# Performance work log

Measured on AMD Instinct MI355X. Metric: run time of the kernel, lower is better.

## Reference

```python
import jax, jax.numpy as jnp
import numpy as np

E, H, D = 512, 8, 64
B, T = 2, 1024
HD = H * D


def _linear(x, W, b):
    return x @ W + b


def _ln(x, g, b):
    mu = x.mean(-1, keepdims=True)
    var = ((x - mu) ** 2).mean(-1, keepdims=True)
    return (x - mu) / jnp.sqrt(var + 1e-5) * g + b


def _l2norm(x):
    n = jnp.sqrt((x * x).sum(-1, keepdims=True))
    return x / jnp.maximum(n, 1e-12)


def setup_inputs() -> dict:
    key = jax.random.key(0)
    ks = jax.random.split(key, 32)
    s = 0.02
    inp = {
        'x': jax.random.normal(ks[0], (B, T, E), jnp.float32),
        'b_min': jax.random.normal(ks[1], (B, T, E), jnp.float32),
        'b_max': jax.random.normal(ks[2], (B, T, E), jnp.float32),
        'motif_context': jax.random.normal(ks[3], (B, T, E), jnp.float32),
        'Wk': jax.random.normal(ks[4], (E, HD), jnp.float32) * s,
        'bk': jnp.zeros((HD,), jnp.float32),
        'Wq': jax.random.normal(ks[5], (E, HD), jnp.float32) * s,
        'bq': jnp.zeros((HD,), jnp.float32),
        'Wv': jax.random.normal(ks[6], (E, HD), jnp.float32) * s,
        'bv': jnp.zeros((HD,), jnp.float32),
        'Wo': jax.random.normal(ks[7], (HD, E), jnp.float32) * s,
        'bo': jnp.zeros((E,), jnp.float32),
        'Wd': jax.random.normal(ks[8], (E, H), jnp.float32) * s,
        'bd': jnp.zeros((H,), jnp.float32),
        'Wgw': jax.random.normal(ks[9], (E, H), jnp.float32) * s,
        'bgw': jnp.zeros((H,), jnp.float32),
        'Wgf': jax.random.normal(ks[10], (E, H), jnp.float32) * s,
        'bgf': jnp.zeros((H,), jnp.float32),
        'Wps': jax.random.normal(ks[11], (E, E), jnp.float32) * s,
        'bps': jnp.zeros((E,), jnp.float32),
        'ln1_g': jnp.ones((E,), jnp.float32),
        'ln1_b': jnp.zeros((E,), jnp.float32),
        'ln2_g': jnp.ones((E,), jnp.float32),
        'ln2_b': jnp.zeros((E,), jnp.float32),
        'W1': jax.random.normal(ks[12], (E, 4 * E), jnp.float32) * s,
        'b1': jnp.zeros((4 * E,), jnp.float32),
        'W2': jax.random.normal(ks[13], (4 * E, E), jnp.float32) * s,
        'b2': jnp.zeros((E,), jnp.float32),
    }
    return inp


def reference(x, b_min, b_max, motif_context,
              Wk, bk, Wq, bq, Wv, bv, Wo, bo, Wd, bd,
              Wgw, bgw, Wgf, bgf, Wps, bps,
              ln1_g, ln1_b, ln2_g, ln2_b, W1, b1, W2, b2):
    Bs, Ts, Es = x.shape
    x_n = _ln(x, ln1_g, ln1_b)
    k = _l2norm(_linear(x_n, Wk, bk).reshape(Bs, Ts, H, D))
    q = _l2norm(_linear(x_n, Wq, bq).reshape(Bs, Ts, H, D))
    v = jnp.tanh(_linear(x_n, Wv, bv).reshape(Bs, Ts, H, D))
    d = jax.nn.softplus(_linear(x_n, Wd, bd))            # (B,T,H)
    gw = jax.nn.sigmoid(_linear(x_n, Wgw, bgw)) ** 2     # (B,T,H)
    gf = 1.0 - jax.nn.sigmoid(_linear(x_n, Wgf, bgf)) ** 2

    # gated linear recurrent scan via cumsum of rank-1 updates
    v_gated = v * (d * gw)[..., None]                    # (B,T,H,D)
    updates = jnp.einsum('bthi,bthj->bthij', v_gated, k)  # (B,T,H,D,D)
    decay = jnp.clip(d * gf, 1e-6, 0.999)
    log_decay = jnp.log(decay)[..., None, None]          # (B,T,H,1,1)
    exp_cum_decay = jnp.exp(jnp.cumsum(log_decay, axis=1))
    state = jnp.cumsum(updates / (exp_cum_decay + 1e-8), axis=1) * exp_cum_decay
    readout = jnp.einsum('bthij,bthj->bthi', state, q)   # (B,T,H,D)
    next_mem = state[:, -1]

    x2 = x + _linear(readout.reshape(Bs, Ts, HD), Wo, bo) + 0.1 * motif_context
    h = _ln(x2, ln2_g, ln2_b)
    x3 = x2 + _linear(jax.nn.gelu(_linear(h, W1, b1), approximate=False), W2, b2)
    probe = _linear(x3, Wps, bps)
    return (x3, next_mem, b_min + probe, b_max + probe)
```

## Files before the change

kernel.cpp:

```cpp
#include <hip/hip_runtime.h>


typedef unsigned short u16;
typedef unsigned int u32;
typedef __attribute__((ext_vector_type(8))) short short8;
typedef __attribute__((ext_vector_type(4))) float floatx4;

__device__ __forceinline__ float b2f(u16 u) {
  u32 x = ((u32)u) << 16;
  return __uint_as_float(x);
}
__device__ __forceinline__ u16 f2b(float f) {
  u32 x = __float_as_uint(f);
  u32 r = (x + 0x7fffu + ((x >> 16) & 1u)) >> 16;
  return (u16)r;
}
__device__ __forceinline__ float4 b4_to_f4(uint2 u) {
  float4 r;
  r.x = __uint_as_float((u.x & 0xffffu) << 16);
  r.y = __uint_as_float(u.x & 0xffff0000u);
  r.z = __uint_as_float((u.y & 0xffffu) << 16);
  r.w = __uint_as_float(u.y & 0xffff0000u);
  return r;
}

__device__ __forceinline__ void stage16(const u16* g, u16* lds_wave_base) {
  __builtin_amdgcn_global_load_lds((const __attribute__((address_space(1))) void*)g,
                                   (__attribute__((address_space(3))) void*)lds_wave_base,
                                   16, 0, 0);
}

template <int ROWS>
__device__ __forceinline__ void stage_tile64(const u16* __restrict__ G, int ldK, int kb,
                                             u16* lds, int tid) {
#pragma unroll
  for (int r = 0; r < ROWS / 32; ++r) {
    int slot = r * 256 + tid;
    int row = slot >> 3;
    int kwg = (slot & 7) ^ (row & 7);
    stage16(G + (size_t)row * ldK + kb * 64 + kwg * 8,
            lds + (size_t)(r * 256 + (tid >> 6) * 64) * 8);
  }
}

__device__ __forceinline__ void ln_row(const float* __restrict__ xr,
                                       const float* __restrict__ g,
                                       const float* __restrict__ bt,
                                       u16* __restrict__ yr, int tid, float* red) {
  float x0 = xr[tid], x1 = xr[tid + 256];
  float s = x0 + x1, ss = x0 * x0 + x1 * x1;
#pragma unroll
  for (int o = 32; o > 0; o >>= 1) { s += __shfl_xor(s, o); ss += __shfl_xor(ss, o); }
  if ((tid & 63) == 0) { red[tid >> 6] = s; red[4 + (tid >> 6)] = ss; }
  __syncthreads();
  float ts = red[0] + red[1] + red[2] + red[3];
  float tss = red[4] + red[5] + red[6] + red[7];
  float mu = ts * (1.f / 512.f);
  float var = tss * (1.f / 512.f) - mu * mu;
  float rstd = 1.0f / sqrtf(var + 1e-5f);
  yr[tid] = f2b((x0 - mu) * rstd * g[tid] + bt[tid]);
  yr[tid + 256] = f2b((x1 - mu) * rstd * g[tid + 256] + bt[tid + 256]);
}

__global__ __launch_bounds__(256) void prep_weights(
    const float* __restrict__ Wk, const float* __restrict__ Wq,
    const float* __restrict__ Wv, const float* __restrict__ Wo,
    const float* __restrict__ Wps, const float* __restrict__ W1,
    const float* __restrict__ W2, const float* __restrict__ Wd,
    const float* __restrict__ Wgw, const float* __restrict__ Wgf,
    const float* __restrict__ bk, const float* __restrict__ bq,
    const float* __restrict__ bv, const float* __restrict__ bd,
    const float* __restrict__ bgw, const float* __restrict__ bgf,
    const float* __restrict__ x, const float* __restrict__ ln1g,
    const float* __restrict__ ln1b,
    u16* __restrict__ WTQ, u16* __restrict__ WTO, u16* __restrict__ WTPS,
    u16* __restrict__ WT1, u16* __restrict__ WT2, float* __restrict__ BQV,
    u16* __restrict__ XN) {
  int bid = blockIdx.x, tid = threadIdx.x;
  __shared__ float tile[32][33];
  __shared__ float red[8];
  if (bid < 3328) {
    const float* src;
    u16* dst;
    int C, rel, tiles_x;
    if (bid < 256)       { src = Wk;  dst = WTQ;           C = 512;  rel = bid;        tiles_x = 16; }
    else if (bid < 512)  { src = Wq;  dst = WTQ + 262144;  C = 512;  rel = bid - 256;  tiles_x = 16; }
    else if (bid < 768)  { src = Wv;  dst = WTQ + 524288;  C = 512;  rel = bid - 512;  tiles_x = 16; }
    else if (bid < 1024) { src = Wo;  dst = WTO;           C = 512;  rel = bid - 768;  tiles_x = 16; }
    else if (bid < 1280) { src = Wps; dst = WTPS;          C = 512;  rel = bid - 1024; tiles_x = 16; }
    else if (bid < 2304) { src = W1;  dst = WT1;           C = 2048; rel = bid - 1280; tiles_x = 64; }
    else                 { src = W2;  dst = WT2;           C = 512;  rel = bid - 2304; tiles_x = 16; }
    int R = (bid >= 1280 && bid < 2304) ? 512 : (bid >= 2304 ? 2048 : 512);
    int c0 = (rel % tiles_x) * 32, r0 = (rel / tiles_x) * 32;
    int tx = tid & 31, ty = tid >> 5;
#pragma unroll
    for (int i = 0; i < 4; ++i)
      tile[ty + i * 8][tx] = src[(size_t)(r0 + ty + i * 8) * C + c0 + tx];
    __syncthreads();
#pragma unroll
    for (int i = 0; i < 4; ++i)
      dst[(size_t)(c0 + ty + i * 8) * R + r0 + tx] = f2b(tile[tx][ty + i * 8]);
  } else if (bid < 3392) {
    int idx = (bid - 3328) * 256 + tid;
    const int stride = 64 * 256;
    for (int i = idx; i < 128 * 512; i += stride) {
      int local = i >> 9, k = i & 511;
      float v = 0.f;
      if (local < 8) v = Wd[k * 8 + local];
      else if (local < 16) v = Wgw[k * 8 + (local - 8)];
      else if (local < 24) v = Wgf[k * 8 + (local - 16)];
      WTQ[(size_t)(1536 + local) * 512 + k] = f2b(v);
    }
    for (int i = idx; i < 1664; i += stride) {
      float v = 0.f;
      if (i < 512) v = bk[i];
      else if (i < 1024) v = bq[i - 512];
      else if (i < 1536) v = bv[i - 1024];
      else if (i < 1544) v = bd[i - 1536];
      else if (i < 1552) v = bgw[i - 1544];
      else if (i < 1560) v = bgf[i - 1552];
      BQV[i] = v;
    }
  } else {
    int row = bid - 3392;
    ln_row(x + (size_t)row * 512, ln1g, ln1b, XN + (size_t)row * 512, tid, red);
  }
}

__global__ __launch_bounds__(256) void ln_f32(const float* __restrict__ X,
                                              const float* __restrict__ g,
                                              const float* __restrict__ bt,
                                              u16* __restrict__ Y) {
  __shared__ float red[8];
  ln_row(X + (size_t)blockIdx.x * 512, g, bt, Y + (size_t)blockIdx.x * 512,
         threadIdx.x, red);
}

template <int BM, int EPI>
__global__ __launch_bounds__(256, (BM == 64 ? 4 : 6)) void gemm2s(
    const u16* __restrict__ A, const u16* __restrict__ BT, const float* __restrict__ bias,
    float* __restrict__ outf, float* __restrict__ outf2, u16* __restrict__ outb,
    u16* __restrict__ outb2, u16* __restrict__ outb3,
    const float* __restrict__ aux0, const float* __restrict__ aux1, int M, int N, int K) {
  constexpr int MT = BM / 32;
  constexpr int S = BM / 32 + 2;
  __shared__ __align__(16) u16 As[2][BM * 64];
  __shared__ __align__(16) u16 Bs[2][64 * 64];
  __shared__ float ssb[2][BM];
  const int tid = threadIdx.x;
  const int lane = tid & 63, wave = tid >> 6;
  const int wm = wave >> 1, wn = wave & 1;
  const int m0 = blockIdx.y * BM, n0 = blockIdx.x * 64;
  floatx4 acc[MT][2] = {};
  const int fr = lane & 15, kq = lane >> 4;
  const int nk = K >> 6;
  const u16* Ab = A + (size_t)m0 * K;
  const u16* Bb = BT + (size_t)n0 * K;

  stage_tile64<BM>(Ab, K, 0, As[0], tid);
  stage_tile64<64>(Bb, K, 0, Bs[0], tid);

  for (int kb = 0; kb < nk; ++kb) {
    const int cur = kb & 1;
    if (kb + 1 < nk) {
      stage_tile64<BM>(Ab, K, kb + 1, As[cur ^ 1], tid);
      stage_tile64<64>(Bb, K, kb + 1, Bs[cur ^ 1], tid);
      if constexpr (S == 4) asm volatile("s_waitcnt vmcnt(4)" ::: "memory");
      else asm volatile("s_waitcnt vmcnt(3)" ::: "memory");
    } else {
      asm volatile("s_waitcnt vmcnt(0)" ::: "memory");
    }
    asm volatile("s_barrier" ::: "memory");

#pragma unroll
    for (int sub = 0; sub < 2; ++sub) {
      short8 af[MT], bf[2];
#pragma unroll
      for (int mt = 0; mt < MT; ++mt) {
        int row = wm * (BM / 2) + mt * 16 + fr;
        int c = sub * 4 + kq;
        af[mt] = *(const short8*)&As[cur][row * 64 + ((c ^ (row & 7)) << 3)];
      }
#pragma unroll
      for (int nt = 0; nt < 2; ++nt) {
        int row = wn * 32 + nt * 16 + fr;
        int c = sub * 4 + kq;
        bf[nt] = *(const short8*)&Bs[cur][row * 64 + ((c ^ (row & 7)) << 3)];
      }
#pragma unroll
      for (int mt = 0; mt < MT; ++mt)
#pragma unroll
        for (int nt = 0; nt < 2; ++nt)
          acc[mt][nt] =
              __builtin_amdgcn_mfma_f32_16x16x32_bf16(af[mt], bf[nt], acc[mt][nt], 0, 0, 0);
    }
    asm volatile("s_waitcnt lgkmcnt(0)" ::: "memory");
    asm volatile("s_barrier" ::: "memory");
  }

  const int col = lane & 15;
  const int rbase = (lane >> 4) * 4;

  float vv[MT][2][4];
#pragma unroll
  for (int nt = 0; nt < 2; ++nt) {
    int gc = n0 + wn * 32 + nt * 16 + col;
    float bvv = bias[gc];
#pragma unroll
    for (int mt = 0; mt < MT; ++mt)
#pragma unroll
      for (int r = 0; r < 4; ++r) vv[mt][nt][r] = acc[mt][nt][r] + bvv;
  }

  if constexpr (EPI == 5) {
    const int sec = n0 >> 9;
    const int h = (n0 & 511) >> 6;
    if (sec == 3) {
#pragma unroll
      for (int nt = 0; nt < 2; ++nt) {
        int gcl = (n0 - 1536) + wn * 32 + nt * 16 + col;
#pragma unroll
        for (int mt = 0; mt < MT; ++mt) {
          int gr = m0 + wm * (BM / 2) + mt * 16 + rbase;
#pragma unroll
          for (int r = 0; r < 4; ++r)
            outf[(size_t)(gr + r) * 128 + gcl] = vv[mt][nt][r];
        }
      }
    } else if (sec == 2) {
#pragma unroll
      for (int nt = 0; nt < 2; ++nt) {
        int d = wn * 32 + nt * 16 + col;
#pragma unroll
        for (int mt = 0; mt < MT; ++mt) {
          int gr = m0 + wm * (BM / 2) + mt * 16 + rbase;
#pragma unroll
          for (int r = 0; r < 4; ++r) {
            int tok = gr + r;
            int bh = (tok >> 10) * 8 + h;
            outb3[((size_t)bh * 1024 + (tok & 1023)) * 64 + d] = f2b(tanhf(vv[mt][nt][r]));
          }
        }
      }
    } else {
#pragma unroll
      for (int mt = 0; mt < MT; ++mt) {
#pragma unroll
        for (int r = 0; r < 4; ++r) {
          float ss = vv[mt][0][r] * vv[mt][0][r] + vv[mt][1][r] * vv[mt][1][r];
          ss += __shfl_xor(ss, 1);
          ss += __shfl_xor(ss, 2);
          ss += __shfl_xor(ss, 4);
          ss += __shfl_xor(ss, 8);
          if ((lane & 15) == 0)
            ssb[wn][wm * (BM / 2) + mt * 16 + rbase + r] = ss;
        }
      }
      __syncthreads();
      u16* dst = (sec == 0) ? outb : outb2;
#pragma unroll
      for (int mt = 0; mt < MT; ++mt) {
#pragma unroll
        for (int r = 0; r < 4; ++r) {
          int br = wm * (BM / 2) + mt * 16 + rbase + r;
          float tot = ssb[0][br] + ssb[1][br];
          float rs = 1.0f / fmaxf(sqrtf(tot), 1e-12f);
          int tok = m0 + br;
          int bh = (tok >> 10) * 8 + h;
          size_t base = ((size_t)bh * 1024 + (tok & 1023)) * 64;
#pragma unroll
          for (int nt = 0; nt < 2; ++nt) {
            int d = wn * 32 + nt * 16 + col;
            dst[base + d] = f2b(vv[mt][nt][r] * rs);
          }
        }
      }
    }
  } else {
#pragma unroll
    for (int nt = 0; nt < 2; ++nt) {
      int gc = n0 + wn * 32 + nt * 16 + col;
#pragma unroll
      for (int mt = 0; mt < MT; ++mt) {
        int gr = m0 + wm * (BM / 2) + mt * 16 + rbase;
#pragma unroll
        for (int r = 0; r < 4; ++r) {
          size_t idx = (size_t)(gr + r) * N + gc;
          float v = vv[mt][nt][r];
          if constexpr (EPI == 1) {
            outf[idx] = aux0[idx] + v + 0.1f * aux1[idx];
          } else if constexpr (EPI == 2) {
            outb[idx] = f2b(0.5f * v * (1.f + erff(v * 0.70710678118654752f)));
          } else if constexpr (EPI == 3) {
            float w = aux0[idx] + v;
            outf[idx] = w;
            outb[idx] = f2b(w);
          } else if constexpr (EPI == 4) {
            outf[idx] = aux0[idx] + v;
            outf2[idx] = aux1[idx] + v;
          }
        }
      }
    }
  }
}

__global__ __launch_bounds__(256) void gates_logcum(
    const float* __restrict__ G0, float* __restrict__ DEC, float* __restrict__ SVG,
    float* __restrict__ LC, float* __restrict__ WW) {
  int bh = blockIdx.x;
  int b = bh >> 3, h = bh & 7;
  int tid = threadIdx.x;
  __shared__ float ldec[1024];
#pragma unroll
  for (int tt = 0; tt < 4; ++tt) {
    int t = tt * 256 + tid;
    size_t tok = (size_t)b * 1024 + t;
    float dl = G0[tok * 128 + h];
    float gwl = G0[tok * 128 + 8 + h];
    float gfl = G0[tok * 128 + 16 + h];
    float dd = dl > 20.f ? dl : log1pf(expf(dl));
    float sw = 1.f / (1.f + expf(-gwl));
    float gw = sw * sw;
    float sf = 1.f / (1.f + expf(-gfl));
    float gf = 1.f - sf * sf;
    float dec = fminf(fmaxf(dd * gf, 1e-6f), 0.999f);
    ldec[t] = dec;
    DEC[(size_t)bh * 1024 + t] = dec;
    SVG[(size_t)bh * 1024 + t] = dd * gw;
  }
  __syncthreads();
  if (tid < 64) {
    int lane = tid;
    size_t base = (size_t)bh * 1024 + lane * 16;
    float loc[16];
    float run = 0.f;
#pragma unroll
    for (int i = 0; i < 16; ++i) { run += logf(ldec[lane * 16 + i]); loc[i] = run; }
    float x = run;
#pragma unroll
    for (int o = 1; o < 64; o <<= 1) {
      float v = __shfl_up(x, o);
      if (lane >= o) x += v;
    }
    float excl = x - run;
#pragma unroll
    for (int i = 0; i < 16; ++i) {
      float L = excl + loc[i];
      LC[base + i] = L;
      float c = expf(L);
      WW[base + i] = c / (c + 1e-8f);
    }
  }
}

__global__ __launch_bounds__(256, 2) void scan_phase1(
    const u16* __restrict__ KB, const u16* __restrict__ QB, const u16* __restrict__ VB,
    const float* __restrict__ DEC, const float* __restrict__ WW,
    const float* __restrict__ SVG, float* __restrict__ RP, float* __restrict__ SF) {
  int chunk = blockIdx.x, h = blockIdx.y, b = blockIdx.z;
  int bh = b * 8 + h;
  int t0 = chunk * 32;
  __shared__ __align__(16) float sk[2048], sq[2048], sv[2048];
  __shared__ float lsa[32], lsw[32];
  int tid = threadIdx.x;

  const u16* gk = KB + ((size_t)bh * 1024 + t0) * 64;
  const u16* gq = QB + ((size_t)bh * 1024 + t0) * 64;
  const u16* gv = VB + ((size_t)bh * 1024 + t0) * 64;
#pragma unroll
  for (int r = 0; r < 2; ++r) {
    int f = (r * 256 + tid) * 4;
    *(float4*)&sk[f] = b4_to_f4(*(const uint2*)(gk + f));
    *(float4*)&sq[f] = b4_to_f4(*(const uint2*)(gq + f));
    *(float4*)&sv[f] = b4_to_f4(*(const uint2*)(gv + f));
  }
  if (tid < 32) {
    size_t gi = (size_t)bh * 1024 + t0 + tid;
    lsa[tid] = DEC[gi];
    lsw[tid] = WW[gi] * SVG[gi];
  }
  __syncthreads();

  int i = tid >> 2, j0 = (tid & 3) * 16;
  float s[16];
#pragma unroll
  for (int z = 0; z < 16; ++z) s[z] = 0.f;

  for (int t = 0; t < 32; ++t) {
    float a = lsa[t], w = lsw[t];
    float wv = w * sv[t * 64 + i];
    float r = 0.f;
#pragma unroll
    for (int u4 = 0; u4 < 4; ++u4) {
      float4 kv = *(const float4*)&sk[t * 64 + j0 + u4 * 4];
      float4 qv = *(const float4*)&sq[t * 64 + j0 + u4 * 4];
      s[u4 * 4 + 0] = fmaf(a, s[u4 * 4 + 0], wv * kv.x); r = fmaf(s[u4 * 4 + 0], qv.x, r);
      s[u4 * 4 + 1] = fmaf(a, s[u4 * 4 + 1], wv * kv.y); r = fmaf(s[u4 * 4 + 1], qv.y, r);
      s[u4 * 4 + 2] = fmaf(a, s[u4 * 4 + 2], wv * kv.z); r = fmaf(s[u4 * 4 + 2], qv.z, r);
      s[u4 * 4 + 3] = fmaf(a, s[u4 * 4 + 3], wv * kv.w); r = fmaf(s[u4 * 4 + 3], qv.w, r);
    }
    r += __shfl_xor(r, 1);
    r += __shfl_xor(r, 2);
    if ((tid & 3) == 0)
      RP[((size_t)(b * 1024 + t0 + t) * 8 + h) * 64 + i] = r;
  }

  float* Sf = SF + ((size_t)bh * 32 + chunk) * 4096 + i * 64 + j0;
#pragma unroll
  for (int u4 = 0; u4 < 4; ++u4) {
    float4 v;
    v.x = s[u4 * 4 + 0]; v.y = s[u4 * 4 + 1]; v.z = s[u4 * 4 + 2]; v.w = s[u4 * 4 + 3];
    *(float4*)&Sf[u4 * 4] = v;
  }
}

__global__ __launch_bounds__(256) void scan_phase2p(const float* __restrict__ SF,
                                                    const float* __restrict__ LC,
                                                    float* __restrict__ SI,
                                                    float* __restrict__ next_mem) {
  int bh = blockIdx.x >> 4;
  int e = (blockIdx.x & 15) * 256 + threadIdx.x;
  float s = 0.f;
  for (int c = 0; c < 32; ++c) {
    SI[((size_t)bh * 32 + c) * 4096 + e] = s;
    float Lend = LC[(size_t)bh * 1024 + c * 32 + 31];
    float Lpre = c ? LC[(size_t)bh * 1024 + c * 32 - 1] : 0.f;
    float P = expf(Lend - Lpre);
    s = fmaf(P, s, SF[((size_t)bh * 32 + c) * 4096 + e]);
  }
  next_mem[(size_t)bh * 4096 + e] = s;
}

__global__ __launch_bounds__(256, 2) void scan_phase3(
    const u16* __restrict__ QB, const float* __restrict__ SI, const float* __restrict__ LC,
    const float* __restrict__ RP, u16* __restrict__ AB) {
  int chunk = blockIdx.x, h = blockIdx.y, b = blockIdx.z;
  int bh = b * 8 + h;
  int t0 = chunk * 32;
  __shared__ __align__(16) float sq[2048];
  __shared__ float sL[32];
  int tid = threadIdx.x;

  const u16* gq = QB + ((size_t)bh * 1024 + t0) * 64;
#pragma unroll
  for (int r = 0; r < 2; ++r) {
    int f = (r * 256 + tid) * 4;
    *(float4*)&sq[f] = b4_to_f4(*(const uint2*)(gq + f));
  }
  if (tid < 32) sL[tid] = LC[(size_t)bh * 1024 + t0 + tid];
  __syncthreads();

  float Lpre = chunk ? LC[(size_t)bh * 1024 + t0 - 1] : 0.f;
  int i = tid >> 2, j0 = (tid & 3) * 16;
  const float* Si = SI + ((size_t)bh * 32 + chunk) * 4096 + i * 64 + j0;
  float S[16];
#pragma unroll
  for (int u4 = 0; u4 < 4; ++u4) {
    float4 v = *(const float4*)&Si[u4 * 4];
    S[u4 * 4 + 0] = v.x; S[u4 * 4 + 1] = v.y; S[u4 * 4 + 2] = v.z; S[u4 * 4 + 3] = v.w;
  }

  for (int t = 0; t < 32; ++t) {
    float p = expf(sL[t] - Lpre);
    float r = 0.f;
#pragma unroll
    for (int u4 = 0; u4 < 4; ++u4) {
      float4 qv = *(const float4*)&sq[t * 64 + j0 + u4 * 4];
      r = fmaf(S[u4 * 4 + 0], qv.x, r);
      r = fmaf(S[u4 * 4 + 1], qv.y, r);
      r = fmaf(S[u4 * 4 + 2], qv.z, r);
      r = fmaf(S[u4 * 4 + 3], qv.w, r);
    }
    r += __shfl_xor(r, 1);
    r += __shfl_xor(r, 2);
    if ((tid & 3) == 0) {
      size_t gi = ((size_t)(b * 1024 + t0 + t) * 8 + h) * 64 + i;
      AB[gi] = f2b(RP[gi] + p * r);
    }
  }
}

extern "C" void kernel_launch(void* const* d_in, const int* in_sizes, int n_in,
                              void* d_out, int out_size, void* d_ws, size_t ws_size,
                              hipStream_t stream) {
  const float* x = (const float*)d_in[0];
  const float* bmin = (const float*)d_in[1];
  const float* bmax = (const float*)d_in[2];
  const float* motif = (const float*)d_in[3];
  const float* Wk = (const float*)d_in[4];
  const float* bk = (const float*)d_in[5];
  const float* Wq = (const float*)d_in[6];
  const float* bq = (const float*)d_in[7];
  const float* Wv = (const float*)d_in[8];
  const float* bv = (const float*)d_in[9];
  const float* Wo = (const float*)d_in[10];
  const float* bo = (const float*)d_in[11];
  const float* Wd = (const float*)d_in[12];
  const float* bd = (const float*)d_in[13];
  const float* Wgw = (const float*)d_in[14];
  const float* bgw = (const float*)d_in[15];
  const float* Wgf = (const float*)d_in[16];
  const float* bgf = (const float*)d_in[17];
  const float* Wps = (const float*)d_in[18];
  const float* bps = (const float*)d_in[19];
  const float* ln1g = (const float*)d_in[20];
  const float* ln1b = (const float*)d_in[21];
  const float* ln2g = (const float*)d_in[22];
  const float* ln2b = (const float*)d_in[23];
  const float* W1 = (const float*)d_in[24];
  const float* b1 = (const float*)d_in[25];
  const float* W2 = (const float*)d_in[26];
  const float* b2 = (const float*)d_in[27];

  char* ws = (char*)d_ws;
  u16* WTQ = (u16*)(ws + 0);
  u16* WTO = (u16*)(ws + 1703936);
  u16* WT1 = (u16*)(ws + 2228224);
  u16* WT2 = (u16*)(ws + 4325376);
  u16* WTPS = (u16*)(ws + 6422528);
  float* BQV = (float*)(ws + 6946816);
  u16* XN = (u16*)(ws + 6953984);
  float* G0 = (float*)(ws + 9051136);
  u16* KB = (u16*)(ws + 10099712);
  u16* QB = (u16*)(ws + 12196864);
  u16* VB = (u16*)(ws + 14294016);
  float* DEC = (float*)(ws + 16391168);
  float* LC = (float*)(ws + 16456704);
  float* WW = (float*)(ws + 16522240);
  float* SVG = (float*)(ws + 16587776);
  float* RP = (float*)(ws + 16653312);
  float* SF = (float*)(ws + 20847616);
  float* SI = (float*)(ws + 29236224);
  u16* AB = (u16*)(ws + 37624832);
  float* X2 = (float*)(ws + 39721984);
  u16* HB = (u16*)(ws + 43916288);
  u16* MID = (u16*)(ws + 9051136);
  u16* X3B = (u16*)(ws + 20847616);

  float* out0 = (float*)d_out;
  float* out1 = out0 + 1048576;
  float* out2 = out0 + 1114112;
  float* out3 = out0 + 2162688;

  prep_weights<<<5440, 256, 0, stream>>>(Wk, Wq, Wv, Wo, Wps, W1, W2, Wd, Wgw, Wgf,
                                         bk, bq, bv, bd, bgw, bgf, x, ln1g, ln1b,
                                         WTQ, WTO, WTPS, WT1, WT2, BQV, XN);
  gemm2s<64, 5><<<dim3(26, 32), 256, 0, stream>>>(XN, WTQ, BQV, G0, nullptr, KB, QB, VB,
                                                  nullptr, nullptr, 2048, 1664, 512);
  gates_logcum<<<16, 256, 0, stream>>>(G0, DEC, SVG, LC, WW);
  scan_phase1<<<dim3(32, 8, 2), 256, 0, stream>>>(KB, QB, VB, DEC, WW, SVG, RP, SF);
  scan_phase2p<<<256, 256, 0, stream>>>(SF, LC, SI, out1);
  scan_phase3<<<dim3(32, 8, 2), 256, 0, stream>>>(QB, SI, LC, RP, AB);

  gemm2s<32, 1><<<dim3(8, 64), 256, 0, stream>>>(AB, WTO, bo, X2, nullptr, nullptr,
                                                 nullptr, nullptr, x, motif, 2048, 512, 512);
  ln_f32<<<2048, 256, 0, stream>>>(X2, ln2g, ln2b, HB);
  gemm2s<64, 2><<<dim3(32, 32), 256, 0, stream>>>(HB, WT1, b1, nullptr, nullptr, MID,
                                                  nullptr, nullptr, nullptr, nullptr,
                                                  2048, 2048, 512);
  gemm2s<32, 3><<<dim3(8, 64), 256, 0, stream>>>(MID, WT2, b2, out0, nullptr, X3B,
                                                 nullptr, nullptr, X2, nullptr,
                                                 2048, 512, 2048);
  gemm2s<32, 4><<<dim3(8, 64), 256, 0, stream>>>(X3B, WTPS, bps, out2, out3, nullptr,
                                                 nullptr, nullptr, bmin, bmax,
                                                 2048, 512, 512);
}
```

Before: 230.3 us.

## Replace LDS-staged GEMMs with single-wave direct-load MFMA GEMMs

```diff
diff --git a/kernel.cpp b/kernel.cpp
--- a/kernel.cpp
+++ b/kernel.cpp
@@ -22,25 +22,6 @@
   r.z = __uint_as_float((u.y & 0xffffu) << 16);
   r.w = __uint_as_float(u.y & 0xffff0000u);
   return r;
-}
-
-__device__ __forceinline__ void stage16(const u16* g, u16* lds_wave_base) {
-  __builtin_amdgcn_global_load_lds((const __attribute__((address_space(1))) void*)g,
-                                   (__attribute__((address_space(3))) void*)lds_wave_base,
-                                   16, 0, 0);
-}
-
-template <int ROWS>
-__device__ __forceinline__ void stage_tile64(const u16* __restrict__ G, int ldK, int kb,
-                                             u16* lds, int tid) {
-#pragma unroll
-  for (int r = 0; r < ROWS / 32; ++r) {
-    int slot = r * 256 + tid;
-    int row = slot >> 3;
-    int kwg = (slot & 7) ^ (row & 7);
-    stage16(G + (size_t)row * ldK + kb * 64 + kwg * 8,
-            lds + (size_t)(r * 256 + (tid >> 6) * 64) * 8);
-  }
 }
 
 __device__ __forceinline__ void ln_row(const float* __restrict__ xr,
@@ -136,75 +117,65 @@
          threadIdx.x, red);
 }
 
-template <int BM, int EPI>
-__global__ __launch_bounds__(256, (BM == 64 ? 4 : 6)) void gemm2s(
+template <int WM, int WN, int EPI>
+__global__ __launch_bounds__(64, 4) void gemm_direct(
     const u16* __restrict__ A, const u16* __restrict__ BT, const float* __restrict__ bias,
     float* __restrict__ outf, float* __restrict__ outf2, u16* __restrict__ outb,
     u16* __restrict__ outb2, u16* __restrict__ outb3,
     const float* __restrict__ aux0, const float* __restrict__ aux1, int M, int N, int K) {
-  constexpr int MT = BM / 32;
-  constexpr int S = BM / 32 + 2;
-  __shared__ __align__(16) u16 As[2][BM * 64];
-  __shared__ __align__(16) u16 Bs[2][64 * 64];
-  __shared__ float ssb[2][BM];
-  const int tid = threadIdx.x;
-  const int lane = tid & 63, wave = tid >> 6;
-  const int wm = wave >> 1, wn = wave & 1;
-  const int m0 = blockIdx.y * BM, n0 = blockIdx.x * 64;
-  floatx4 acc[MT][2] = {};
+  constexpr int MT = WM / 16, NT = WN / 16;
+  const int lane = threadIdx.x;
   const int fr = lane & 15, kq = lane >> 4;
-  const int nk = K >> 6;
-  const u16* Ab = A + (size_t)m0 * K;
-  const u16* Bb = BT + (size_t)n0 * K;
-
-  stage_tile64<BM>(Ab, K, 0, As[0], tid);
-  stage_tile64<64>(Bb, K, 0, Bs[0], tid);
-
-  for (int kb = 0; kb < nk; ++kb) {
-    const int cur = kb & 1;
-    if (kb + 1 < nk) {
-      stage_tile64<BM>(Ab, K, kb + 1, As[cur ^ 1], tid);
-      stage_tile64<64>(Bb, K, kb + 1, Bs[cur ^ 1], tid);
-      if constexpr (S == 4) asm volatile("s_waitcnt vmcnt(4)" ::: "memory");
-      else asm volatile("s_waitcnt vmcnt(3)" ::: "memory");
-    } else {
-      asm volatile("s_waitcnt vmcnt(0)" ::: "memory");
-    }
-    asm volatile("s_barrier" ::: "memory");
-
-#pragma unroll
-    for (int sub = 0; sub < 2; ++sub) {
-      short8 af[MT], bf[2];
-#pragma unroll
-      for (int mt = 0; mt < MT; ++mt) {
-        int row = wm * (BM / 2) + mt * 16 + fr;
-        int c = sub * 4 + kq;
-        af[mt] = *(const short8*)&As[cur][row * 64 + ((c ^ (row & 7)) << 3)];
-      }
-#pragma unroll
-      for (int nt = 0; nt < 2; ++nt) {
-        int row = wn * 32 + nt * 16 + fr;
-        int c = sub * 4 + kq;
-        bf[nt] = *(const short8*)&Bs[cur][row * 64 + ((c ^ (row & 7)) << 3)];
-      }
-#pragma unroll
-      for (int mt = 0; mt < MT; ++mt)
-#pragma unroll
-        for (int nt = 0; nt < 2; ++nt)
-          acc[mt][nt] =
-              __builtin_amdgcn_mfma_f32_16x16x32_bf16(af[mt], bf[nt], acc[mt][nt], 0, 0, 0);
-    }
-    asm volatile("s_waitcnt lgkmcnt(0)" ::: "memory");
-    asm volatile("s_barrier" ::: "memory");
-  }
+  const int m0 = blockIdx.y * WM, n0 = blockIdx.x * WN;
+
+  const u16* ap[MT];
+  const u16* bp[NT];
+#pragma unroll
+  for (int mt = 0; mt < MT; ++mt)
+    ap[mt] = A + (size_t)(m0 + mt * 16 + fr) * K + kq * 8;
+#pragma unroll
+  for (int nt = 0; nt < NT; ++nt)
+    bp[nt] = BT + (size_t)(n0 + nt * 16 + fr) * K + kq * 8;
+
+  floatx4 acc[MT][NT] = {};
+  const int nk = K >> 5;
+  short8 af[MT], bf[NT], afn[MT], bfn[NT];
+#pragma unroll
+  for (int mt = 0; mt < MT; ++mt) af[mt] = *(const short8*)(ap[mt]);
+#pragma unroll
+  for (int nt = 0; nt < NT; ++nt) bf[nt] = *(const short8*)(bp[nt]);
+
+#pragma unroll 2
+  for (int kb = 0; kb < nk - 1; ++kb) {
+#pragma unroll
+    for (int mt = 0; mt < MT; ++mt) afn[mt] = *(const short8*)(ap[mt] + (kb + 1) * 32);
+#pragma unroll
+    for (int nt = 0; nt < NT; ++nt) bfn[nt] = *(const short8*)(bp[nt] + (kb + 1) * 32);
+#pragma unroll
+    for (int mt = 0; mt < MT; ++mt)
+#pragma unroll
+      for (int nt = 0; nt < NT; ++nt)
+        acc[mt][nt] =
+            __builtin_amdgcn_mfma_f32_16x16x32_bf16(af[mt], bf[nt], acc[mt][nt], 0, 0, 0);
+#pragma unroll
+    for (int mt = 0; mt < MT; ++mt) af[mt] = afn[mt];
+#pragma unroll
+    for (int nt = 0; nt < NT; ++nt) bf[nt] = bfn[nt];
+  }
+#pragma unroll
+  for (int mt = 0; mt < MT; ++mt)
+#pragma unroll
+    for (int nt = 0; nt < NT; ++nt)
+      acc[mt][nt] =
+          __builtin_amdgcn_mfma_f32_16x16x32_bf16(af[mt], bf[nt], acc[mt][nt], 0, 0, 0);
 
   const int col = lane & 15;
   const int rbase = (lane >> 4) * 4;
 
-  float vv[MT][2][4];
-#pragma unroll
-  for (int nt = 0; nt < 2; ++nt) {
-    int gc = n0 + wn * 32 + nt * 16 + col;
+  float vv[MT][NT][4];
+#pragma unroll
+  for (int nt = 0; nt < NT; ++nt) {
+    int gc = n0 + nt * 16 + col;
     float bvv = bias[gc];
 #pragma unroll
     for (int mt = 0; mt < MT; ++mt)
@@ -217,11 +188,11 @@
     const int h = (n0 & 511) >> 6;
     if (sec == 3) {
 #pragma unroll
-      for (int nt = 0; nt < 2; ++nt) {
-        int gcl = (n0 - 1536) + wn * 32 + nt * 16 + col;
+      for (int nt = 0; nt < NT; ++nt) {
+        int gcl = (n0 - 1536) + nt * 16 + col;
 #pragma unroll
         for (int mt = 0; mt < MT; ++mt) {
-          int gr = m0 + wm * (BM / 2) + mt * 16 + rbase;
+          int gr = m0 + mt * 16 + rbase;
 #pragma unroll
           for (int r = 0; r < 4; ++r)
             outf[(size_t)(gr + r) * 128 + gcl] = vv[mt][nt][r];
@@ -229,60 +200,50 @@
       }
     } else if (sec == 2) {
 #pragma unroll
-      for (int nt = 0; nt < 2; ++nt) {
-        int d = wn * 32 + nt * 16 + col;
+      for (int nt = 0; nt < NT; ++nt) {
+        int d = nt * 16 + col;
 #pragma unroll
         for (int mt = 0; mt < MT; ++mt) {
-          int gr = m0 + wm * (BM / 2) + mt * 16 + rbase;
+          int gr = m0 + mt * 16 + rbase;
 #pragma unroll
           for (int r = 0; r < 4; ++r) {
             int tok = gr + r;
             int bh = (tok >> 10) * 8 + h;
-            outb3[((size_t)bh * 1024 + (tok & 1023)) * 64 + d] = f2b(tanhf(vv[mt][nt][r]));
+            outb3[((size_t)bh * 1024 + (tok & 1023)) * 64 + d] =
+                f2b(tanhf(vv[mt][nt][r]));
           }
         }
       }
     } else {
+      u16* dst = (sec == 0) ? outb : outb2;
 #pragma unroll
       for (int mt = 0; mt < MT; ++mt) {
 #pragma unroll
         for (int r = 0; r < 4; ++r) {
-          float ss = vv[mt][0][r] * vv[mt][0][r] + vv[mt][1][r] * vv[mt][1][r];
+          float ss = 0.f;
+#pragma unroll
+          for (int nt = 0; nt < NT; ++nt) ss += vv[mt][nt][r] * vv[mt][nt][r];
           ss += __shfl_xor(ss, 1);
           ss += __shfl_xor(ss, 2);
           ss += __shfl_xor(ss, 4);
           ss += __shfl_xor(ss, 8);
-          if ((lane & 15) == 0)
-            ssb[wn][wm * (BM / 2) + mt * 16 + rbase + r] = ss;
+          float rs = 1.0f / fmaxf(sqrtf(ss), 1e-12f);
+          int tok = m0 + mt * 16 + rbase + r;
+          int bh = (tok >> 10) * 8 + h;
+          size_t base = ((size_t)bh * 1024 + (tok & 1023)) * 64;
+#pragma unroll
+          for (int nt = 0; nt < NT; ++nt)
+            dst[base + nt * 16 + col] = f2b(vv[mt][nt][r] * rs);
         }
       }
-      __syncthreads();
-      u16* dst = (sec == 0) ? outb : outb2;
+    }
+  } else {
+#pragma unroll
+    for (int nt = 0; nt < NT; ++nt) {
+      int gc = n0 + nt * 16 + col;
 #pragma unroll
       for (int mt = 0; mt < MT; ++mt) {
-#pragma unroll
-        for (int r = 0; r < 4; ++r) {
-          int br = wm * (BM / 2) + mt * 16 + rbase + r;
-          float tot = ssb[0][br] + ssb[1][br];
-          float rs = 1.0f / fmaxf(sqrtf(tot), 1e-12f);
-          int tok = m0 + br;
-          int bh = (tok >> 10) * 8 + h;
-          size_t base = ((size_t)bh * 1024 + (tok & 1023)) * 64;
-#pragma unroll
-          for (int nt = 0; nt < 2; ++nt) {
-            int d = wn * 32 + nt * 16 + col;
-            dst[base + d] = f2b(vv[mt][nt][r] * rs);
-          }
-        }
-      }
-    }
-  } else {
-#pragma unroll
-    for (int nt = 0; nt < 2; ++nt) {
-      int gc = n0 + wn * 32 + nt * 16 + col;
-#pragma unroll
-      for (int mt = 0; mt < MT; ++mt) {
-        int gr = m0 + wm * (BM / 2) + mt * 16 + rbase;
+        int gr = m0 + mt * 16 + rbase;
 #pragma unroll
         for (int r = 0; r < 4; ++r) {
           size_t idx = (size_t)(gr + r) * N + gc;
@@ -546,23 +507,23 @@
   prep_weights<<<5440, 256, 0, stream>>>(Wk, Wq, Wv, Wo, Wps, W1, W2, Wd, Wgw, Wgf,
                                          bk, bq, bv, bd, bgw, bgf, x, ln1g, ln1b,
                                          WTQ, WTO, WTPS, WT1, WT2, BQV, XN);
-  gemm2s<64, 5><<<dim3(26, 32), 256, 0, stream>>>(XN, WTQ, BQV, G0, nullptr, KB, QB, VB,
-                                                  nullptr, nullptr, 2048, 1664, 512);
+  gemm_direct<32, 64, 5><<<dim3(26, 64), 64, 0, stream>>>(
+      XN, WTQ, BQV, G0, nullptr, KB, QB, VB, nullptr, nullptr, 2048, 1664, 512);
   gates_logcum<<<16, 256, 0, stream>>>(G0, DEC, SVG, LC, WW);
   scan_phase1<<<dim3(32, 8, 2), 256, 0, stream>>>(KB, QB, VB, DEC, WW, SVG, RP, SF);
   scan_phase2p<<<256, 256, 0, stream>>>(SF, LC, SI, out1);
   scan_phase3<<<dim3(32, 8, 2), 256, 0, stream>>>(QB, SI, LC, RP, AB);
 
-  gemm2s<32, 1><<<dim3(8, 64), 256, 0, stream>>>(AB, WTO, bo, X2, nullptr, nullptr,
-                                                 nullptr, nullptr, x, motif, 2048, 512, 512);
+  gemm_direct<16, 32, 1><<<dim3(16, 128), 64, 0, stream>>>(
+      AB, WTO, bo, X2, nullptr, nullptr, nullptr, nullptr, x, motif, 2048, 512, 512);
   ln_f32<<<2048, 256, 0, stream>>>(X2, ln2g, ln2b, HB);
-  gemm2s<64, 2><<<dim3(32, 32), 256, 0, stream>>>(HB, WT1, b1, nullptr, nullptr, MID,
-                                                  nullptr, nullptr, nullptr, nullptr,
-                                                  2048, 2048, 512);
-  gemm2s<32, 3><<<dim3(8, 64), 256, 0, stream>>>(MID, WT2, b2, out0, nullptr, X3B,
-                                                 nullptr, nullptr, X2, nullptr,
-                                                 2048, 512, 2048);
-  gemm2s<32, 4><<<dim3(8, 64), 256, 0, stream>>>(X3B, WTPS, bps, out2, out3, nullptr,
-                                                 nullptr, nullptr, bmin, bmax,
-                                                 2048, 512, 512);
-}
+  gemm_direct<32, 32, 2><<<dim3(64, 64), 64, 0, stream>>>(
+      HB, WT1, b1, nullptr, nullptr, MID, nullptr, nullptr, nullptr, nullptr,
+      2048, 2048, 512);
+  gemm_direct<16, 32, 3><<<dim3(16, 128), 64, 0, stream>>>(
+      MID, WT2, b2, out0, nullptr, X3B, nullptr, nullptr, X2, nullptr,
+      2048, 512, 2048);
+  gemm_direct<16, 32, 4><<<dim3(16, 128), 64, 0, stream>>>(
+      X3B, WTPS, bps, out2, out3, nullptr, nullptr, nullptr, bmin, bmax,
+      2048, 512, 512);
+}
```

After: 300.6 us. 1.31x slower.

## Use 4-stage K=32 pipelined GEMM for BM=64 kernels, specialize BM=32 GEMM

Applied to the files above, without the earlier changes.

```diff
diff --git a/kernel.cpp b/kernel.cpp
--- a/kernel.cpp
+++ b/kernel.cpp
@@ -41,6 +41,14 @@
     stage16(G + (size_t)row * ldK + kb * 64 + kwg * 8,
             lds + (size_t)(r * 256 + (tid >> 6) * 64) * 8);
   }
+}
+
+__device__ __forceinline__ void stage_tile32(const u16* __restrict__ G, int ldK, int kb,
+                                             u16* lds, int tid) {
+  int row = tid >> 2;
+  int kwg = (tid & 3) ^ ((row >> 1) & 3);
+  stage16(G + (size_t)row * ldK + kb * 32 + kwg * 8,
+          lds + (size_t)((tid >> 6) * 64) * 8);
 }
 
 __device__ __forceinline__ void ln_row(const float* __restrict__ xr,
@@ -136,78 +144,76 @@
          threadIdx.x, red);
 }
 
-template <int BM, int EPI>
-__global__ __launch_bounds__(256, (BM == 64 ? 4 : 6)) void gemm2s(
+template <int EPI>
+__global__ __launch_bounds__(256, 4) void gemm4s(
     const u16* __restrict__ A, const u16* __restrict__ BT, const float* __restrict__ bias,
-    float* __restrict__ outf, float* __restrict__ outf2, u16* __restrict__ outb,
-    u16* __restrict__ outb2, u16* __restrict__ outb3,
-    const float* __restrict__ aux0, const float* __restrict__ aux1, int M, int N, int K) {
-  constexpr int MT = BM / 32;
-  constexpr int S = BM / 32 + 2;
-  __shared__ __align__(16) u16 As[2][BM * 64];
-  __shared__ __align__(16) u16 Bs[2][64 * 64];
-  __shared__ float ssb[2][BM];
+    float* __restrict__ outf, u16* __restrict__ outb, u16* __restrict__ outb2,
+    u16* __restrict__ outb3, int M, int N, int K) {
+  __shared__ __align__(16) u16 As[4][64 * 32];
+  __shared__ __align__(16) u16 Bs[4][64 * 32];
+  __shared__ float ssb[2][64];
   const int tid = threadIdx.x;
   const int lane = tid & 63, wave = tid >> 6;
   const int wm = wave >> 1, wn = wave & 1;
-  const int m0 = blockIdx.y * BM, n0 = blockIdx.x * 64;
-  floatx4 acc[MT][2] = {};
+  const int m0 = blockIdx.y * 64, n0 = blockIdx.x * 64;
+  floatx4 acc[2][2] = {};
   const int fr = lane & 15, kq = lane >> 4;
-  const int nk = K >> 6;
+  const int nk = K >> 5;
   const u16* Ab = A + (size_t)m0 * K;
   const u16* Bb = BT + (size_t)n0 * K;
 
-  stage_tile64<BM>(Ab, K, 0, As[0], tid);
-  stage_tile64<64>(Bb, K, 0, Bs[0], tid);
+  stage_tile32(Ab, K, 0, As[0], tid);
+  stage_tile32(Bb, K, 0, Bs[0], tid);
+  stage_tile32(Ab, K, 1, As[1], tid);
+  stage_tile32(Bb, K, 1, Bs[1], tid);
+  stage_tile32(Ab, K, 2, As[2], tid);
+  stage_tile32(Bb, K, 2, Bs[2], tid);
 
   for (int kb = 0; kb < nk; ++kb) {
-    const int cur = kb & 1;
-    if (kb + 1 < nk) {
-      stage_tile64<BM>(Ab, K, kb + 1, As[cur ^ 1], tid);
-      stage_tile64<64>(Bb, K, kb + 1, Bs[cur ^ 1], tid);
-      if constexpr (S == 4) asm volatile("s_waitcnt vmcnt(4)" ::: "memory");
-      else asm volatile("s_waitcnt vmcnt(3)" ::: "memory");
-    } else {
-      asm volatile("s_waitcnt vmcnt(0)" ::: "memory");
-    }
+    const int cur = kb & 3;
+    if (kb + 3 < nk) {
+      const int nxt = (kb + 3) & 3;
+      stage_tile32(Ab, K, kb + 3, As[nxt], tid);
+      stage_tile32(Bb, K, kb + 3, Bs[nxt], tid);
+    }
+    int ahead = nk - 1 - kb;
+    if (ahead > 3) ahead = 3;
+    if (ahead == 3) asm volatile("s_waitcnt vmcnt(6)" ::: "memory");
+    else if (ahead == 2) asm volatile("s_waitcnt vmcnt(4)" ::: "memory");
+    else if (ahead == 1) asm volatile("s_waitcnt vmcnt(2)" ::: "memory");
+    else asm volatile("s_waitcnt vmcnt(0)" ::: "memory");
     asm volatile("s_barrier" ::: "memory");
 
-#pragma unroll
-    for (int sub = 0; sub < 2; ++sub) {
-      short8 af[MT], bf[2];
-#pragma unroll
-      for (int mt = 0; mt < MT; ++mt) {
-        int row = wm * (BM / 2) + mt * 16 + fr;
-        int c = sub * 4 + kq;
-        af[mt] = *(const short8*)&As[cur][row * 64 + ((c ^ (row & 7)) << 3)];
-      }
-#pragma unroll
-      for (int nt = 0; nt < 2; ++nt) {
-        int row = wn * 32 + nt * 16 + fr;
-        int c = sub * 4 + kq;
-        bf[nt] = *(const short8*)&Bs[cur][row * 64 + ((c ^ (row & 7)) << 3)];
-      }
-#pragma unroll
-      for (int mt = 0; mt < MT; ++mt)
-#pragma unroll
-        for (int nt = 0; nt < 2; ++nt)
-          acc[mt][nt] =
-              __builtin_amdgcn_mfma_f32_16x16x32_bf16(af[mt], bf[nt], acc[mt][nt], 0, 0, 0);
-    }
+    short8 af[2], bf[2];
+#pragma unroll
+    for (int mt = 0; mt < 2; ++mt) {
+      int row = wm * 32 + mt * 16 + fr;
+      af[mt] = *(const short8*)&As[cur][row * 32 + ((kq ^ ((row >> 1) & 3)) << 3)];
+    }
+#pragma unroll
+    for (int nt = 0; nt < 2; ++nt) {
+      int row = wn * 32 + nt * 16 + fr;
+      bf[nt] = *(const short8*)&Bs[cur][row * 32 + ((kq ^ ((row >> 1) & 3)) << 3)];
+    }
+#pragma unroll
+    for (int mt = 0; mt < 2; ++mt)
+#pragma unroll
+      for (int nt = 0; nt < 2; ++nt)
+        acc[mt][nt] =
+            __builtin_amdgcn_mfma_f32_16x16x32_bf16(af[mt], bf[nt], acc[mt][nt], 0, 0, 0);
     asm volatile("s_waitcnt lgkmcnt(0)" ::: "memory");
     asm volatile("s_barrier" ::: "memory");
   }
 
   const int col = lane & 15;
   const int rbase = (lane >> 4) * 4;
-
-  float vv[MT][2][4];
+  float vv[2][2][4];
 #pragma unroll
   for (int nt = 0; nt < 2; ++nt) {
     int gc = n0 + wn * 32 + nt * 16 + col;
     float bvv = bias[gc];
 #pragma unroll
-    for (int mt = 0; mt < MT; ++mt)
+    for (int mt = 0; mt < 2; ++mt)
 #pragma unroll
       for (int r = 0; r < 4; ++r) vv[mt][nt][r] = acc[mt][nt][r] + bvv;
   }
@@ -220,8 +226,8 @@
       for (int nt = 0; nt < 2; ++nt) {
         int gcl = (n0 - 1536) + wn * 32 + nt * 16 + col;
 #pragma unroll
-        for (int mt = 0; mt < MT; ++mt) {
-          int gr = m0 + wm * (BM / 2) + mt * 16 + rbase;
+        for (int mt = 0; mt < 2; ++mt) {
+          int gr = m0 + wm * 32 + mt * 16 + rbase;
 #pragma unroll
           for (int r = 0; r < 4; ++r)
             outf[(size_t)(gr + r) * 128 + gcl] = vv[mt][nt][r];
@@ -232,19 +238,20 @@
       for (int nt = 0; nt < 2; ++nt) {
         int d = wn * 32 + nt * 16 + col;
 #pragma unroll
-        for (int mt = 0; mt < MT; ++mt) {
-          int gr = m0 + wm * (BM / 2) + mt * 16 + rbase;
+        for (int mt = 0; mt < 2; ++mt) {
+          int gr = m0 + wm * 32 + mt * 16 + rbase;
 #pragma unroll
           for (int r = 0; r < 4; ++r) {
             int tok = gr + r;
             int bh = (tok >> 10) * 8 + h;
-            outb3[((size_t)bh * 1024 + (tok & 1023)) * 64 + d] = f2b(tanhf(vv[mt][nt][r]));
+            outb3[((size_t)bh * 1024 + (tok & 1023)) * 64 + d] =
+                f2b(tanhf(vv[mt][nt][r]));
           }
         }
       }
     } else {
 #pragma unroll
-      for (int mt = 0; mt < MT; ++mt) {
+      for (int mt = 0; mt < 2; ++mt) {
 #pragma unroll
         for (int r = 0; r < 4; ++r) {
           float ss = vv[mt][0][r] * vv[mt][0][r] + vv[mt][1][r] * vv[mt][1][r];
@@ -252,17 +259,16 @@
           ss += __shfl_xor(ss, 2);
           ss += __shfl_xor(ss, 4);
           ss += __shfl_xor(ss, 8);
-          if ((lane & 15) == 0)
-            ssb[wn][wm * (BM / 2) + mt * 16 + rbase + r] = ss;
+          if ((lane & 15) == 0) ssb[wn][wm * 32 + mt * 16 + rbase + r] = ss;
         }
       }
       __syncthreads();
       u16* dst = (sec == 0) ? outb : outb2;
 #pragma unroll
-      for (int mt = 0; mt < MT; ++mt) {
+      for (int mt = 0; mt < 2; ++mt) {
 #pragma unroll
         for (int r = 0; r < 4; ++r) {
-          int br = wm * (BM / 2) + mt * 16 + rbase + r;
+          int br = wm * 32 + mt * 16 + rbase + r;
           float tot = ssb[0][br] + ssb[1][br];
           float rs = 1.0f / fmaxf(sqrtf(tot), 1e-12f);
           int tok = m0 + br;
@@ -281,25 +287,92 @@
     for (int nt = 0; nt < 2; ++nt) {
       int gc = n0 + wn * 32 + nt * 16 + col;
 #pragma unroll
-      for (int mt = 0; mt < MT; ++mt) {
-        int gr = m0 + wm * (BM / 2) + mt * 16 + rbase;
+      for (int mt = 0; mt < 2; ++mt) {
+        int gr = m0 + wm * 32 + mt * 16 + rbase;
 #pragma unroll
         for (int r = 0; r < 4; ++r) {
           size_t idx = (size_t)(gr + r) * N + gc;
           float v = vv[mt][nt][r];
-          if constexpr (EPI == 1) {
-            outf[idx] = aux0[idx] + v + 0.1f * aux1[idx];
-          } else if constexpr (EPI == 2) {
-            outb[idx] = f2b(0.5f * v * (1.f + erff(v * 0.70710678118654752f)));
-          } else if constexpr (EPI == 3) {
-            float w = aux0[idx] + v;
-            outf[idx] = w;
-            outb[idx] = f2b(w);
-          } else if constexpr (EPI == 4) {
-            outf[idx] = aux0[idx] + v;
-            outf2[idx] = aux1[idx] + v;
-          }
+          outb[idx] = f2b(0.5f * v * (1.f + erff(v * 0.70710678118654752f)));
         }
+      }
+    }
+  }
+}
+
+template <int EPI>
+__global__ __launch_bounds__(256, 6) void gemm2s(
+    const u16* __restrict__ A, const u16* __restrict__ BT, const float* __restrict__ bias,
+    float* __restrict__ outf, float* __restrict__ outf2, u16* __restrict__ outb,
+    const float* __restrict__ aux0, const float* __restrict__ aux1, int M, int N, int K) {
+  __shared__ __align__(16) u16 As[2][32 * 64];
+  __shared__ __align__(16) u16 Bs[2][64 * 64];
+  const int tid = threadIdx.x;
+  const int lane = tid & 63, wave = tid >> 6;
+  const int wm = wave >> 1, wn = wave & 1;
+  const int m0 = blockIdx.y * 32, n0 = blockIdx.x * 64;
+  floatx4 acc[2] = {};
+  const int fr = lane & 15, kq = lane >> 4;
+  const int nk = K >> 6;
+  const u16* Ab = A + (size_t)m0 * K;
+  const u16* Bb = BT + (size_t)n0 * K;
+
+  stage_tile64<32>(Ab, K, 0, As[0], tid);
+  stage_tile64<64>(Bb, K, 0, Bs[0], tid);
+
+  for (int kb = 0; kb < nk; ++kb) {
+    const int cur = kb & 1;
+    if (kb + 1 < nk) {
+      stage_tile64<32>(Ab, K, kb + 1, As[cur ^ 1], tid);
+      stage_tile64<64>(Bb, K, kb + 1, Bs[cur ^ 1], tid);
+      asm volatile("s_waitcnt vmcnt(3)" ::: "memory");
+    } else {
+      asm volatile("s_waitcnt vmcnt(0)" ::: "memory");
+    }
+    asm volatile("s_barrier" ::: "memory");
+
+#pragma unroll
+    for (int sub = 0; sub < 2; ++sub) {
+      short8 af, bf[2];
+      {
+        int row = wm * 16 + fr;
+        int c = sub * 4 + kq;
+        af = *(const short8*)&As[cur][row * 64 + ((c ^ (row & 7)) << 3)];
+      }
+#pragma unroll
+      for (int nt = 0; nt < 2; ++nt) {
+        int row = wn * 32 + nt * 16 + fr;
+        int c = sub * 4 + kq;
+        bf[nt] = *(const short8*)&Bs[cur][row * 64 + ((c ^ (row & 7)) << 3)];
+      }
+#pragma unroll
+      for (int nt = 0; nt < 2; ++nt)
+        acc[nt] = __builtin_amdgcn_mfma_f32_16x16x32_bf16(af, bf[nt], acc[nt], 0, 0, 0);
+    }
+    asm volatile("s_waitcnt lgkmcnt(0)" ::: "memory");
+    asm volatile("s_barrier" ::: "memory");
+  }
+
+  const int col = lane & 15;
+  const int rbase = (lane >> 4) * 4;
+#pragma unroll
+  for (int nt = 0; nt < 2; ++nt) {
+    int gc = n0 + wn * 32 + nt * 16 + col;
+    float bvv = bias[gc];
+    int gr = m0 + wm * 16 + rbase;
+#pragma unroll
+    for (int r = 0; r < 4; ++r) {
+      size_t idx = (size_t)(gr + r) * N + gc;
+      float v = acc[nt][r] + bvv;
+      if constexpr (EPI == 1) {
+        outf[idx] = aux0[idx] + v + 0.1f * aux1[idx];
+      } else if constexpr (EPI == 3) {
+        float w = aux0[idx] + v;
+        outf[idx] = w;
+        outb[idx] = f2b(w);
+      } else if constexpr (EPI == 4) {
+        outf[idx] = aux0[idx] + v;
+        outf2[idx] = aux1[idx] + v;
       }
     }
   }
@@ -546,23 +619,20 @@
   prep_weights<<<5440, 256, 0, stream>>>(Wk, Wq, Wv, Wo, Wps, W1, W2, Wd, Wgw, Wgf,
                                          bk, bq, bv, bd, bgw, bgf, x, ln1g, ln1b,
                                          WTQ, WTO, WTPS, WT1, WT2, BQV, XN);
-  gemm2s<64, 5><<<dim3(26, 32), 256, 0, stream>>>(XN, WTQ, BQV, G0, nullptr, KB, QB, VB,
-                                                  nullptr, nullptr, 2048, 1664, 512);
+  gemm4s<5><<<dim3(26, 32), 256, 0, stream>>>(XN, WTQ, BQV, G0, KB, QB, VB,
+                                              2048, 1664, 512);
   gates_logcum<<<16, 256, 0, stream>>>(G0, DEC, SVG, LC, WW);
   scan_phase1<<<dim3(32, 8, 2), 256, 0, stream>>>(KB, QB, VB, DEC, WW, SVG, RP, SF);
   scan_phase2p<<<256, 256, 0, stream>>>(SF, LC, SI, out1);
   scan_phase3<<<dim3(32, 8, 2), 256, 0, stream>>>(QB, SI, LC, RP, AB);
 
-  gemm2s<32, 1><<<dim3(8, 64), 256, 0, stream>>>(AB, WTO, bo, X2, nullptr, nullptr,
-                                                 nullptr, nullptr, x, motif, 2048, 512, 512);
+  gemm2s<1><<<dim3(8, 64), 256, 0, stream>>>(AB, WTO, bo, X2, nullptr, nullptr,
+                                             x, motif, 2048, 512, 512);
   ln_f32<<<2048, 256, 0, stream>>>(X2, ln2g, ln2b, HB);
-  gemm2s<64, 2><<<dim3(32, 32), 256, 0, stream>>>(HB, WT1, b1, nullptr, nullptr, MID,
-                                                  nullptr, nullptr, nullptr, nullptr,
-                                                  2048, 2048, 512);
-  gemm2s<32, 3><<<dim3(8, 64), 256, 0, stream>>>(MID, WT2, b2, out0, nullptr, X3B,
-                                                 nullptr, nullptr, X2, nullptr,
-                                                 2048, 512, 2048);
-  gemm2s<32, 4><<<dim3(8, 64), 256, 0, stream>>>(X3B, WTPS, bps, out2, out3, nullptr,
-                                                 nullptr, nullptr, bmin, bmax,
-                                                 2048, 512, 512);
-}
+  gemm4s<2><<<dim3(32, 32), 256, 0, stream>>>(HB, WT1, b1, nullptr, MID, nullptr,
+                                              nullptr, 2048, 2048, 512);
+  gemm2s<3><<<dim3(8, 64), 256, 0, stream>>>(MID, WT2, b2, out0, nullptr, X3B,
+                                             X2, nullptr, 2048, 512, 2048);
+  gemm2s<4><<<dim3(8, 64), 256, 0, stream>>>(X3B, WTPS, bps, out2, out3, nullptr,
+                                             bmin, bmax, 2048, 512, 512);
+}
```

New measurement: 233.4 us. About the same (+1.4%).
